# Kernel tuning notes

Hardware: AMD Instinct MI355X
Metric: run time of the kernel (lower is better)

Reference implementation:

```python
import jax, jax.numpy as jnp
import numpy as np

B = 16        # graphs per batch
NPG = 4096    # nodes per graph
N = B * NPG
EPG = 32768   # edges per graph
E = B * EPG
F_NODE, F_EDGE, G, H, A = 8, 4, 16, 128, 10


def setup_inputs() -> dict:
    key = jax.random.key(0)
    ks = jax.random.split(key, 32)
    x = jax.random.normal(ks[0], (N, F_NODE), jnp.float32)
    # random intra-graph edges, offset into the batched node id space
    src = jax.random.randint(ks[1], (B, EPG), 0, NPG)
    dst = jax.random.randint(ks[2], (B, EPG), 0, NPG)
    off = (jnp.arange(B) * NPG)[:, None]
    edge_index = jnp.stack([(src + off).reshape(-1), (dst + off).reshape(-1)]).astype(jnp.int64)
    edge_attr = jax.random.normal(ks[3], (E, F_EDGE), jnp.float32)
    global_state = jax.random.normal(ks[4], (B, G), jnp.float32)
    current_pipe_nodes = jax.random.randint(ks[5], (B, 2), 0, NPG).astype(jnp.int64)

    def w(k, shape):
        fan_in = shape[0] if len(shape) > 1 else shape[0]
        return jax.random.normal(k, shape, jnp.float32) * (1.0 / np.sqrt(fan_in))

    return dict(
        x=x, edge_index=edge_index, edge_attr=edge_attr,
        global_state=global_state, current_pipe_nodes=current_pipe_nodes,
        W_l1=w(ks[6], (F_NODE, H)), W_r1=w(ks[7], (F_NODE, H)), W_e1=w(ks[8], (F_EDGE, H)),
        att1=w(ks[9], (H,)), b1=jnp.zeros((H,), jnp.float32),
        W_l2=w(ks[10], (H, H)), W_r2=w(ks[11], (H, H)), W_e2=w(ks[12], (F_EDGE, H)),
        att2=w(ks[13], (H,)), b2=jnp.zeros((H,), jnp.float32),
        W_c=w(ks[14], (H + 2 * H + G, 256)), b_c=jnp.zeros((256,), jnp.float32),
        W_a1=w(ks[15], (256, 128)), b_a1=jnp.zeros((128,), jnp.float32),
        W_a2=w(ks[16], (128, A)), b_a2=jnp.zeros((A,), jnp.float32),
        W_v1=w(ks[17], (256, 128)), b_v1=jnp.zeros((128,), jnp.float32),
        W_v2=w(ks[18], (128, 1)), b_v2=jnp.zeros((1,), jnp.float32),
    )


def add_self_loops(edge_index, edge_attr, n):
    # PyG default: add_self_loops=True, fill_value='mean' -> loop attr is the
    # mean of incoming edge_attr per node (zeros if none).
    dst = edge_index[1]
    deg = jax.ops.segment_sum(jnp.ones(dst.shape, jnp.float32), dst, num_segments=n)
    loop_attr = jax.ops.segment_sum(edge_attr, dst, num_segments=n) / jnp.maximum(deg, 1.0)[:, None]
    loops = jnp.tile(jnp.arange(n, dtype=edge_index.dtype)[None, :], (2, 1))
    ei = jnp.concatenate([edge_index, loops], axis=1)
    ea = jnp.concatenate([edge_attr, loop_attr], axis=0)
    return ei, ea


def gatv2(x, ei, ea, Wl, Wr, We, att, bias, n):
    # GATv2Conv (heads=1): score = att . leaky_relu(Wl x_j + Wr x_i + We e_ij)
    # message = alpha_ij * (Wl x_j); segment softmax over incoming edges of i.
    src, dst = ei[0], ei[1]
    xl = x @ Wl                                   # [N,H]
    xr = x @ Wr                                   # [N,H]
    m = xl[src] + xr[dst] + ea @ We               # [E,H]
    s = jax.nn.leaky_relu(m, 0.2) @ att           # [E]
    smax = jax.ops.segment_max(s, dst, num_segments=n)
    ealpha = jnp.exp(s - smax[dst])
    denom = jax.ops.segment_sum(ealpha, dst, num_segments=n)
    alpha = ealpha / denom[dst]
    out = jax.ops.segment_sum(alpha[:, None] * xl[src], dst, num_segments=n)
    return out + bias


def reference(x, edge_index, edge_attr, global_state, current_pipe_nodes,
              W_l1, W_r1, W_e1, att1, b1,
              W_l2, W_r2, W_e2, att2, b2,
              W_c, b_c, W_a1, b_a1, W_a2, b_a2, W_v1, b_v1, W_v2, b_v2):
    ei, ea = add_self_loops(edge_index, edge_attr, N)
    h = jax.nn.relu(gatv2(x, ei, ea, W_l1, W_r1, W_e1, att1, b1, N))
    h = gatv2(h, ei, ea, W_l2, W_r2, W_e2, att2, b2, N)
    # global_mean_pool: graphs are contiguous equal-size blocks
    graph_emb = h.reshape(B, NPG, H).mean(axis=1)                       # [B,H]
    abs_idx = current_pipe_nodes + (jnp.arange(B) * NPG)[:, None]       # [B,2]
    pipe_emb = h[abs_idx.reshape(-1)].reshape(B, 2 * H)                 # [B,2H]
    comb = jnp.concatenate([graph_emb, pipe_emb, global_state], axis=1)
    feat = jax.nn.relu(comb @ W_c + b_c)
    logits = jax.nn.relu(feat @ W_a1 + b_a1) @ W_a2 + b_a2              # [B,A]
    value = jax.nn.relu(feat @ W_v1 + b_v1) @ W_v2 + b_v2               # [B,1]
    return jnp.concatenate([logits, value], axis=1)                     # [B,A+1]
```

## Files before the change

kernel.cpp:

```cpp
#include <hip/hip_runtime.h>
#include <math.h>

#define NN   65536
#define NPG  4096
#define NB   16
#define NE   524288
#define EPG  32768
#define SB   8
#define NH   128
#define FN   8
#define FE   4
#define NG   16
#define NA   10
#define NFRAG 2048

typedef __attribute__((ext_vector_type(8))) short bf16x8;
typedef __attribute__((ext_vector_type(4))) float f32x4;

static __device__ __forceinline__ short bf16rne(float f) {
    unsigned u = __builtin_bit_cast(unsigned, f);
    u += 0x7FFFu + ((u >> 16) & 1u);
    return (short)(u >> 16);
}

__global__ void hist_lin1_kernel(const int* __restrict__ ei, int* __restrict__ subhist,
                                 const float* __restrict__ x,
                                 const float* __restrict__ Wl, const float* __restrict__ Wr,
                                 float* __restrict__ xl, float* __restrict__ xr) {
    int bid = blockIdx.x;
    if (bid < NB * SB) {
        __shared__ int hh[NPG];
        int g = bid >> 3, sb = bid & 7;
        int t = threadIdx.x;
        for (int i = t; i < NPG; i += 256) hh[i] = 0;
        __syncthreads();
        const int* dstp = ei + NE + g * EPG + sb * (EPG / SB);
        for (int i = t; i < EPG / SB; i += 256)
            atomicAdd(&hh[dstp[i] - g * NPG], 1);
        __syncthreads();
        int* out = subhist + (size_t)bid * NPG;
        for (int i = t; i < NPG; i += 256) out[i] = hh[i];
    } else {
        __shared__ float row[2][FN];
        int b2 = bid - NB * SB;
        int sub = threadIdx.x >> 7;
        int k = threadIdx.x & 127;
        int n = b2 * 2 + sub;
        if (k < FN) row[sub][k] = x[n * FN + k];
        __syncthreads();
        float al = 0.f, ar = 0.f;
#pragma unroll
        for (int j = 0; j < FN; ++j) {
            float v = row[sub][j];
            al += v * Wl[j * NH + k];
            ar += v * Wr[j * NH + k];
        }
        xl[n * NH + k] = al;
        xr[n * NH + k] = ar;
    }
}

__global__ __launch_bounds__(1024) void scan_kernel(
        const int* __restrict__ subhist, int* __restrict__ offs, int* __restrict__ cur2,
        const float* __restrict__ Wl2, const float* __restrict__ Wr2,
        bf16x8* __restrict__ wbf) {
    int g = blockIdx.x, t = threadIdx.x;
    if (g >= NB) {
        int sel = g - NB;
        const float* W = sel ? Wr2 : Wl2;
#pragma unroll
        for (int q = 0; q < 2; ++q) {
            int f = t * 2 + q;
            int lane = f & 63;
            int kgct = f >> 6;
            int kg = kgct & 3, ct = kgct >> 2;
            int kbase = kg * 32 + (lane >> 4) * 8;
            int c = ct * 16 + (lane & 15);
            bf16x8 v;
#pragma unroll
            for (int j = 0; j < 8; ++j)
                v[j] = bf16rne(W[(kbase + j) * NH + c]);
            wbf[sel * NFRAG + f] = v;
        }
        return;
    }
    __shared__ int psum[1024];
    int h[4][SB];
    int loc[4];
    int run = 0;
#pragma unroll
    for (int i = 0; i < 4; ++i) {
        int nl = t * 4 + i;
        int d = 0;
#pragma unroll
        for (int sb = 0; sb < SB; ++sb) {
            int v = subhist[((size_t)(g * SB + sb)) * NPG + nl];
            h[i][sb] = v;
            d += v;
        }
        loc[i] = run;
        run += d;
    }
    psum[t] = run;
    __syncthreads();
    for (int s = 1; s < 1024; s <<= 1) {
        int add = (t >= s) ? psum[t - s] : 0;
        __syncthreads();
        psum[t] += add;
        __syncthreads();
    }
    int prefix = (t == 0) ? 0 : psum[t - 1];
    int ebase = g * EPG;
#pragma unroll
    for (int i = 0; i < 4; ++i) {
        int nl = t * 4 + i;
        int off = ebase + prefix + loc[i];
        offs[g * NPG + nl] = off;
        int running = off;
#pragma unroll
        for (int sb = 0; sb < SB; ++sb) {
            cur2[((size_t)(g * SB + sb)) * NPG + nl] = running;
            running += h[i][sb];
        }
    }
    if (g == NB - 1 && t == 0) offs[NN] = NE;
}

__global__ __launch_bounds__(1024) void csr_fill_kernel(
        const int* __restrict__ ei, const int* __restrict__ cur2, int2* __restrict__ csr) {
    __shared__ int cur[NPG];
    int bid = blockIdx.x;
    int g = bid >> 3, sb = bid & 7;
    int t = threadIdx.x;
    const int* base = cur2 + (size_t)bid * NPG;
    for (int i = t; i < NPG; i += 1024) cur[i] = base[i];
    __syncthreads();
    int e0 = g * EPG + sb * (EPG / SB);
#pragma unroll
    for (int i = 0; i < (EPG / SB) / 1024; ++i) {
        int e = e0 + i * 1024 + t;
        int dst = ei[NE + e];
        int src = ei[e];
        int pos = atomicAdd(&cur[dst - g * NPG], 1);
        csr[pos] = make_int2(src, e);
    }
}

__global__ __launch_bounds__(256) void gat_gather_kernel(
        const float4* __restrict__ xl, const float4* __restrict__ xr,
        const float4* __restrict__ ea,
        const int2* __restrict__ csr, const int* __restrict__ offs,
        const float* __restrict__ We, const float* __restrict__ att,
        const float* __restrict__ bias, float* __restrict__ out,
        unsigned short* __restrict__ hbf_out,
        float4* __restrict__ lattr_w, const float4* __restrict__ lattr_r,
        float4* __restrict__ gpart, int do_relu) {
    __shared__ float4 red[8][32];
    int grp = threadIdx.x >> 5;
    int lane = threadIdx.x & 31;
    int bid = blockIdx.x;
    int xcd = bid & 7, slot = bid >> 3;
    int g = xcd + ((slot >> 9) << 3);
    int blk = slot & 511;
    int node = g * NPG + blk * 8 + grp;

    float4 xr4 = xr[node * 32 + lane];
    float4 att4 = ((const float4*)att)[lane];
    const float4* We4 = (const float4*)We;
    float4 we0 = We4[lane];
    float4 we1 = We4[32 + lane];
    float4 we2 = We4[64 + lane];
    float4 we3 = We4[96 + lane];

    int beg = offs[node], end = offs[node + 1];
    float l = 0.f;
    float4 acc = make_float4(0.f, 0.f, 0.f, 0.f);
    float4 easum = make_float4(0.f, 0.f, 0.f, 0.f);
    bool have_lattr = (lattr_r != nullptr);
    if (beg < end) {
        int last = end - 1;
        int2 se0 = csr[beg];
        int p1 = (beg + 1 <= last) ? beg + 1 : last;
        int2 se1 = csr[p1];
        float4 xl0 = xl[se0.x * 32 + lane];
        float4 a0 = ea[se0.y];
        for (int p = beg; p < end; ++p) {
            int p2 = (p + 2 <= last) ? p + 2 : last;
            int2 se2 = csr[p2];
            float4 xl1 = xl[se1.x * 32 + lane];
            float4 a1 = ea[se1.y];
            if (!have_lattr) {
                easum.x += a0.x; easum.y += a0.y; easum.z += a0.z; easum.w += a0.w;
            }
            float tx = xl0.x + xr4.x + a0.x * we0.x + a0.y * we1.x + a0.z * we2.x + a0.w * we3.x;
            float ty = xl0.y + xr4.y + a0.x * we0.y + a0.y * we1.y + a0.z * we2.y + a0.w * we3.y;
            float tz = xl0.z + xr4.z + a0.x * we0.z + a0.y * we1.z + a0.z * we2.z + a0.w * we3.z;
            float tw = xl0.w + xr4.w + a0.x * we0.w + a0.y * we1.w + a0.z * we2.w + a0.w * we3.w;
            tx = tx > 0.f ? tx : 0.2f * tx;
            ty = ty > 0.f ? ty : 0.2f * ty;
            tz = tz > 0.f ? tz : 0.2f * tz;
            tw = tw > 0.f ? tw : 0.2f * tw;
            float s = tx * att4.x + ty * att4.y + tz * att4.z + tw * att4.w;
#pragma unroll
            for (int o = 16; o >= 1; o >>= 1) s += __shfl_xor(s, o);
            float w = __expf(s);
            l += w;
            acc.x += w * xl0.x;
            acc.y += w * xl0.y;
            acc.z += w * xl0.z;
            acc.w += w * xl0.w;
            se1 = se2; xl0 = xl1; a0 = a1;
        }
    }
    {
        float ax, ay, az, aw;
        if (have_lattr) {
            float4 la = lattr_r[node];
            ax = la.x; ay = la.y; az = la.z; aw = la.w;
        } else {
            int deg = end - beg;
            float invd = 1.0f / (float)(deg > 0 ? deg : 1);
            ax = easum.x * invd; ay = easum.y * invd;
            az = easum.z * invd; aw = easum.w * invd;
            if (lane == 0) lattr_w[node] = make_float4(ax, ay, az, aw);
        }
        float4 xl4 = xl[node * 32 + lane];
        float tx = xl4.x + xr4.x + ax * we0.x + ay * we1.x + az * we2.x + aw * we3.x;
        float ty = xl4.y + xr4.y + ax * we0.y + ay * we1.y + az * we2.y + aw * we3.y;
        float tz = xl4.z + xr4.z + ax * we0.z + ay * we1.z + az * we2.z + aw * we3.z;
        float tw = xl4.w + xr4.w + ax * we0.w + ay * we1.w + az * we2.w + aw * we3.w;
        tx = tx > 0.f ? tx : 0.2f * tx;
        ty = ty > 0.f ? ty : 0.2f * ty;
        tz = tz > 0.f ? tz : 0.2f * tz;
        tw = tw > 0.f ? tw : 0.2f * tw;
        float s = tx * att4.x + ty * att4.y + tz * att4.z + tw * att4.w;
#pragma unroll
        for (int o = 16; o >= 1; o >>= 1) s += __shfl_xor(s, o);
        float w = __expf(s);
        l += w;
        acc.x += w * xl4.x;
        acc.y += w * xl4.y;
        acc.z += w * xl4.z;
        acc.w += w * xl4.w;
    }
    float inv = 1.0f / l;
    float4 b4 = ((const float4*)bias)[lane];
    float4 o4;
    o4.x = acc.x * inv + b4.x;
    o4.y = acc.y * inv + b4.y;
    o4.z = acc.z * inv + b4.z;
    o4.w = acc.w * inv + b4.w;
    if (do_relu) {
        o4.x = fmaxf(o4.x, 0.f); o4.y = fmaxf(o4.y, 0.f);
        o4.z = fmaxf(o4.z, 0.f); o4.w = fmaxf(o4.w, 0.f);
    }
    if (hbf_out != nullptr) {
        int rt = node >> 4, m = node & 15;
        int kg = lane >> 3, qd = (lane & 7) >> 1, j0 = (lane & 1) * 4;
        ushort4 v;
        v.x = (unsigned short)bf16rne(o4.x);
        v.y = (unsigned short)bf16rne(o4.y);
        v.z = (unsigned short)bf16rne(o4.z);
        v.w = (unsigned short)bf16rne(o4.w);
        *(ushort4*)&hbf_out[(size_t)(((rt * 4 + kg) * 64 + qd * 16 + m)) * 8 + j0] = v;
    } else {
        ((float4*)out)[node * 32 + lane] = o4;
    }

    if (gpart != nullptr) {
        red[grp][lane] = o4;
        __syncthreads();
        if (grp < 4) {
            float4 o = red[grp + 4][lane];
            red[grp][lane] = make_float4(red[grp][lane].x + o.x, red[grp][lane].y + o.y,
                                         red[grp][lane].z + o.z, red[grp][lane].w + o.w);
        }
        __syncthreads();
        if (grp < 2) {
            float4 o = red[grp + 2][lane];
            red[grp][lane] = make_float4(red[grp][lane].x + o.x, red[grp][lane].y + o.y,
                                         red[grp][lane].z + o.z, red[grp][lane].w + o.w);
        }
        __syncthreads();
        if (grp == 0) {
            float4 a = red[0][lane], b = red[1][lane];
            gpart[(g * 512 + blk) * 32 + lane] =
                make_float4(a.x + b.x, a.y + b.y, a.z + b.z, a.w + b.w);
        }
    }
}

__global__ __launch_bounds__(256) void lin2_mfma_kernel(
        const bf16x8* __restrict__ hbf, const bf16x8* __restrict__ wbf,
        float* __restrict__ xl, float* __restrict__ xr) {
    const bf16x8* Bf = wbf + (size_t)blockIdx.y * NFRAG;
    float* C = blockIdx.y ? xr : xl;
    int t = threadIdx.x;
    int wv = t >> 6, lane = t & 63;
    int rt = blockIdx.x * 4 + wv;
    int row0 = rt * 16;
    int m = lane & 15, qd = lane >> 4;
    bf16x8 afrag[4];
#pragma unroll
    for (int kg = 0; kg < 4; ++kg)
        afrag[kg] = hbf[(size_t)(rt * 4 + kg) * 64 + lane];
#pragma unroll
    for (int ct = 0; ct < 8; ++ct) {
        f32x4 acc = {0.f, 0.f, 0.f, 0.f};
#pragma unroll
        for (int kg = 0; kg < 4; ++kg) {
            bf16x8 b = Bf[((ct << 2) | kg) * 64 + lane];
            acc = __builtin_amdgcn_mfma_f32_16x16x32_bf16(afrag[kg], b, acc, 0, 0, 0);
        }
        int col = ct * 16 + m;
#pragma unroll
        for (int r = 0; r < 4; ++r)
            C[(size_t)(row0 + qd * 4 + r) * NH + col] = acc[r];
    }
}

__global__ __launch_bounds__(1024) void head_kernel(
        const float* __restrict__ gpart, const float* __restrict__ h,
        const float* __restrict__ gstate, const int* __restrict__ cpn,
        const float* __restrict__ Wc, const float* __restrict__ bc,
        const float* __restrict__ Wa1, const float* __restrict__ ba1,
        const float* __restrict__ Wa2, const float* __restrict__ ba2,
        const float* __restrict__ Wv1, const float* __restrict__ bv1,
        const float* __restrict__ Wv2, const float* __restrict__ bv2,
        float* __restrict__ out) {
    int b = blockIdx.x, t = threadIdx.x;
    __shared__ float comb[400];
    __shared__ float part[4][256];
    __shared__ float pp[8][128];
    __shared__ float feat[256];
    __shared__ float hid[256];
    int n0 = cpn[b * 2 + 0] + b * NPG;
    int n1 = cpn[b * 2 + 1] + b * NPG;
    {
        int d = t & 127, p = t >> 7;
        const float* gp = gpart + (size_t)b * 512 * NH + d;
        float s = 0.f;
        int c0 = p * 64;
        for (int c = c0; c < c0 + 64; ++c) s += gp[c * NH];
        pp[p][d] = s;
    }
    if (t >= 128 && t < 256) comb[128 + (t - 128)] = h[(size_t)n0 * NH + (t - 128)];
    else if (t >= 256 && t < 384) comb[t] = h[(size_t)n1 * NH + (t - 256)];
    else if (t >= 384 && t < 400) comb[t] = gstate[b * NG + (t - 384)];
    __syncthreads();
    if (t < 128) {
        float s = pp[0][t] + pp[1][t] + pp[2][t] + pp[3][t]
                + pp[4][t] + pp[5][t] + pp[6][t] + pp[7][t];
        comb[t] = s * (1.0f / NPG);
    }
    __syncthreads();
    {
        int col = t & 255, p = t >> 8;
        float a = 0.f;
        int j0 = p * 100;
        for (int j = j0; j < j0 + 100; ++j) a += comb[j] * Wc[j * 256 + col];
        part[p][col] = a;
    }
    __syncthreads();
    if (t < 256)
        feat[t] = fmaxf(bc[t] + part[0][t] + part[1][t] + part[2][t] + part[3][t], 0.f);
    __syncthreads();
    {
        int col = t & 255, p = t >> 8;
        const float* W = (col < 128) ? Wa1 : Wv1;
        int cc = col & 127;
        float a = 0.f;
        int j0 = p * 64;
        for (int j = j0; j < j0 + 64; ++j) a += feat[j] * W[j * 128 + cc];
        part[p][col] = a;
    }
    __syncthreads();
    if (t < 256) {
        float bias = (t < 128) ? ba1[t] : bv1[t - 128];
        hid[t] = fmaxf(bias + part[0][t] + part[1][t] + part[2][t] + part[3][t], 0.f);
    }
    __syncthreads();
    if (t < NA) {
        float a2 = ba2[t];
        for (int j = 0; j < NH; ++j) a2 += hid[j] * Wa2[j * NA + t];
        out[b * 11 + t] = a2;
    } else if (t == NA) {
        float a2 = bv2[0];
        for (int j = 0; j < NH; ++j) a2 += hid[128 + j] * Wv2[j];
        out[b * 11 + 10] = a2;
    }
}

extern "C" void kernel_launch(void* const* d_in, const int* in_sizes, int n_in,
                              void* d_out, int out_size, void* d_ws, size_t ws_size,
                              hipStream_t stream) {
    const float* x      = (const float*)d_in[0];
    const int*   ei     = (const int*)d_in[1];
    const float* ea     = (const float*)d_in[2];
    const float* gstate = (const float*)d_in[3];
    const int*   cpn    = (const int*)d_in[4];
    const float* Wl1 = (const float*)d_in[5];
    const float* Wr1 = (const float*)d_in[6];
    const float* We1 = (const float*)d_in[7];
    const float* att1= (const float*)d_in[8];
    const float* b1  = (const float*)d_in[9];
    const float* Wl2 = (const float*)d_in[10];
    const float* Wr2 = (const float*)d_in[11];
    const float* We2 = (const float*)d_in[12];
    const float* att2= (const float*)d_in[13];
    const float* b2  = (const float*)d_in[14];
    const float* Wc  = (const float*)d_in[15];
    const float* bc  = (const float*)d_in[16];
    const float* Wa1 = (const float*)d_in[17];
    const float* ba1 = (const float*)d_in[18];
    const float* Wa2 = (const float*)d_in[19];
    const float* ba2 = (const float*)d_in[20];
    const float* Wv1 = (const float*)d_in[21];
    const float* bv1 = (const float*)d_in[22];
    const float* Wv2 = (const float*)d_in[23];
    const float* bv2 = (const float*)d_in[24];

    char* ws = (char*)d_ws;
    size_t o = 0;
    float* xl     = (float*)(ws + o); o += (size_t)NN * NH * 4;
    float* xr     = (float*)(ws + o); o += (size_t)NN * NH * 4;
    float* h      = (float*)(ws + o); o += (size_t)NN * NH * 4;
    unsigned short* hbf = (unsigned short*)(ws + o); o += (size_t)NN * NH * 2;
    float* lattr  = (float*)(ws + o); o += (size_t)NN * 16;
    float* gpart  = (float*)(ws + o); o += (size_t)NB * 512 * NH * 4;
    int*   offs   = (int*)(ws + o);   o += (((size_t)(NN + 1) * 4 + 255) & ~(size_t)255);
    int*   subhist= (int*)(ws + o);   o += (size_t)NB * SB * NPG * 4;
    int*   cur2   = (int*)(ws + o);   o += (size_t)NB * SB * NPG * 4;
    int2*  csr    = (int2*)(ws + o);  o += (size_t)NE * 8;
    bf16x8* wbf   = (bf16x8*)(ws + o); o += (size_t)2 * NFRAG * 16;
    (void)o; (void)ws_size; (void)in_sizes; (void)n_in; (void)out_size;

    hist_lin1_kernel<<<NB * SB + NN / 2, 256, 0, stream>>>(ei, subhist, x, Wl1, Wr1, xl, xr);
    scan_kernel<<<NB + 2, 1024, 0, stream>>>(subhist, offs, cur2, Wl2, Wr2, wbf);
    csr_fill_kernel<<<NB * SB, 1024, 0, stream>>>(ei, cur2, csr);
    gat_gather_kernel<<<NN / 8, 256, 0, stream>>>((const float4*)xl, (const float4*)xr,
        (const float4*)ea, csr, offs, We1, att1, b1, nullptr, hbf,
        (float4*)lattr, nullptr, nullptr, 1);
    lin2_mfma_kernel<<<dim3(NN / 64, 2), 256, 0, stream>>>((const bf16x8*)hbf, wbf, xl, xr);
    gat_gather_kernel<<<NN / 8, 256, 0, stream>>>((const float4*)xl, (const float4*)xr,
        (const float4*)ea, csr, offs, We2, att2, b2, h, nullptr,
        nullptr, (const float4*)lattr, (float4*)gpart, 0);
    head_kernel<<<NB, 1024, 0, stream>>>(gpart, h, gstate, cpn, Wc, bc, Wa1, ba1, Wa2, ba2,
                                         Wv1, bv1, Wv2, bv2, (float*)d_out);
}
```

Measured before the change: 296.2 us.

## Fuse scan into CSR fill, move weight packing, write only pipe-node rows

Removes the separate scan kernel. Each csr_fill block now recomputes its graph's prefix scan and its own sub-block cursor offsets, and the bf16 weight packing moves into two extra blocks of the histogram kernel. The second GAT layer no longer writes the full 32 MB fp32 h array. It stores only the two pipe-node rows per graph, which the head kernel reads. This trades one launch and a large global write for redundant scan work (8x per graph) inside csr_fill.

```diff
diff --git a/kernel.cpp b/kernel.cpp
--- a/kernel.cpp
+++ b/kernel.cpp
@@ -26,6 +26,8 @@
 __global__ void hist_lin1_kernel(const int* __restrict__ ei, int* __restrict__ subhist,
                                  const float* __restrict__ x,
                                  const float* __restrict__ Wl, const float* __restrict__ Wr,
+                                 const float* __restrict__ Wl2, const float* __restrict__ Wr2,
+                                 bf16x8* __restrict__ wbf,
                                  float* __restrict__ xl, float* __restrict__ xr) {
     int bid = blockIdx.x;
     if (bid < NB * SB) {
@@ -40,37 +42,13 @@
         __syncthreads();
         int* out = subhist + (size_t)bid * NPG;
         for (int i = t; i < NPG; i += 256) out[i] = hh[i];
-    } else {
-        __shared__ float row[2][FN];
-        int b2 = bid - NB * SB;
-        int sub = threadIdx.x >> 7;
-        int k = threadIdx.x & 127;
-        int n = b2 * 2 + sub;
-        if (k < FN) row[sub][k] = x[n * FN + k];
-        __syncthreads();
-        float al = 0.f, ar = 0.f;
-#pragma unroll
-        for (int j = 0; j < FN; ++j) {
-            float v = row[sub][j];
-            al += v * Wl[j * NH + k];
-            ar += v * Wr[j * NH + k];
-        }
-        xl[n * NH + k] = al;
-        xr[n * NH + k] = ar;
-    }
-}
-
-__global__ __launch_bounds__(1024) void scan_kernel(
-        const int* __restrict__ subhist, int* __restrict__ offs, int* __restrict__ cur2,
-        const float* __restrict__ Wl2, const float* __restrict__ Wr2,
-        bf16x8* __restrict__ wbf) {
-    int g = blockIdx.x, t = threadIdx.x;
-    if (g >= NB) {
-        int sel = g - NB;
+    } else if (bid < NB * SB + 2) {
+        int sel = bid - NB * SB;
         const float* W = sel ? Wr2 : Wl2;
-#pragma unroll
-        for (int q = 0; q < 2; ++q) {
-            int f = t * 2 + q;
+        int t = threadIdx.x;
+#pragma unroll
+        for (int q = 0; q < 8; ++q) {
+            int f = t * 8 + q;
             int lane = f & 63;
             int kgct = f >> 6;
             int kg = kgct & 3, ct = kgct >> 2;
@@ -82,58 +60,69 @@
                 v[j] = bf16rne(W[(kbase + j) * NH + c]);
             wbf[sel * NFRAG + f] = v;
         }
-        return;
-    }
+    } else {
+        __shared__ float row[2][FN];
+        int b2 = bid - NB * SB - 2;
+        int sub = threadIdx.x >> 7;
+        int k = threadIdx.x & 127;
+        int n = b2 * 2 + sub;
+        if (k < FN) row[sub][k] = x[n * FN + k];
+        __syncthreads();
+        float al = 0.f, ar = 0.f;
+#pragma unroll
+        for (int j = 0; j < FN; ++j) {
+            float v = row[sub][j];
+            al += v * Wl[j * NH + k];
+            ar += v * Wr[j * NH + k];
+        }
+        xl[n * NH + k] = al;
+        xr[n * NH + k] = ar;
+    }
+}
+
+__global__ __launch_bounds__(1024) void csr_fill_kernel(
+        const int* __restrict__ ei, const int* __restrict__ subhist,
+        int* __restrict__ offs, int2* __restrict__ csr) {
+    __shared__ int cur[NPG];
     __shared__ int psum[1024];
-    int h[4][SB];
-    int loc[4];
-    int run = 0;
-#pragma unroll
-    for (int i = 0; i < 4; ++i) {
-        int nl = t * 4 + i;
-        int d = 0;
-#pragma unroll
-        for (int sb = 0; sb < SB; ++sb) {
-            int v = subhist[((size_t)(g * SB + sb)) * NPG + nl];
-            h[i][sb] = v;
-            d += v;
-        }
-        loc[i] = run;
-        run += d;
-    }
-    psum[t] = run;
-    __syncthreads();
-    for (int s = 1; s < 1024; s <<= 1) {
-        int add = (t >= s) ? psum[t - s] : 0;
-        __syncthreads();
-        psum[t] += add;
-        __syncthreads();
-    }
-    int prefix = (t == 0) ? 0 : psum[t - 1];
-    int ebase = g * EPG;
-#pragma unroll
-    for (int i = 0; i < 4; ++i) {
-        int nl = t * 4 + i;
-        int off = ebase + prefix + loc[i];
-        offs[g * NPG + nl] = off;
-        int running = off;
-#pragma unroll
-        for (int sb = 0; sb < SB; ++sb) {
-            cur2[((size_t)(g * SB + sb)) * NPG + nl] = running;
-            running += h[i][sb];
-        }
-    }
-    if (g == NB - 1 && t == 0) offs[NN] = NE;
-}
-
-__global__ __launch_bounds__(1024) void csr_fill_kernel(
-        const int* __restrict__ ei, const int* __restrict__ cur2, int2* __restrict__ csr) {
-    __shared__ int cur[NPG];
     int bid = blockIdx.x;
     int g = bid >> 3, sb = bid & 7;
     int t = threadIdx.x;
-    const int* base = cur2 + (size_t)bid * NPG;
-    for (int i = t; i < NPG; i += 1024) cur[i] = base[i];
+    int base4 = t * 4;
+    int dpre[4], loc[4];
+    int run = 0;
+#pragma unroll
+    for (int i = 0; i < 4; ++i) {
+        int nl = base4 + i;
+        int d = 0, pre = 0;
+#pragma unroll
+        for (int s = 0; s < SB; ++s) {
+            int v = subhist[((size_t)(g * SB + s)) * NPG + nl];
+            pre += (s < sb) ? v : 0;
+            d += v;
+        }
+        dpre[i] = pre;
+        loc[i] = run;
+        run += d;
+    }
+    psum[t] = run;
+    __syncthreads();
+    for (int s = 1; s < 1024; s <<= 1) {
+        int add = (t >= s) ? psum[t - s] : 0;
+        __syncthreads();
+        psum[t] += add;
+        __syncthreads();
+    }
+    int prefix = (t == 0) ? 0 : psum[t - 1];
+    int ebase = g * EPG;
+#pragma unroll
+    for (int i = 0; i < 4; ++i) {
+        int nl = base4 + i;
+        int off = ebase + prefix + loc[i];
+        cur[nl] = off + dpre[i];
+        if (sb == 0) offs[g * NPG + nl] = off;
+    }
+    if (sb == 0 && g == NB - 1 && t == 0) offs[NN] = NE;
     __syncthreads();
     int e0 = g * EPG + sb * (EPG / SB);
 #pragma unroll
@@ -151,10 +140,11 @@
         const float4* __restrict__ ea,
         const int2* __restrict__ csr, const int* __restrict__ offs,
         const float* __restrict__ We, const float* __restrict__ att,
-        const float* __restrict__ bias, float* __restrict__ out,
+        const float* __restrict__ bias,
         unsigned short* __restrict__ hbf_out,
         float4* __restrict__ lattr_w, const float4* __restrict__ lattr_r,
-        float4* __restrict__ gpart, int do_relu) {
+        float4* __restrict__ gpart, float4* __restrict__ pipe,
+        const int* __restrict__ cpn, int do_relu) {
     __shared__ float4 red[8][32];
     int grp = threadIdx.x >> 5;
     int lane = threadIdx.x & 31;
@@ -264,7 +254,9 @@
         v.w = (unsigned short)bf16rne(o4.w);
         *(ushort4*)&hbf_out[(size_t)(((rt * 4 + kg) * 64 + qd * 16 + m)) * 8 + j0] = v;
     } else {
-        ((float4*)out)[node * 32 + lane] = o4;
+        int nl = node - g * NPG;
+        if (nl == cpn[g * 2 + 0]) pipe[(g * 2 + 0) * 32 + lane] = o4;
+        if (nl == cpn[g * 2 + 1]) pipe[(g * 2 + 1) * 32 + lane] = o4;
     }
 
     if (gpart != nullptr) {
@@ -320,8 +312,8 @@
 }
 
 __global__ __launch_bounds__(1024) void head_kernel(
-        const float* __restrict__ gpart, const float* __restrict__ h,
-        const float* __restrict__ gstate, const int* __restrict__ cpn,
+        const float* __restrict__ gpart, const float* __restrict__ pipe,
+        const float* __restrict__ gstate,
         const float* __restrict__ Wc, const float* __restrict__ bc,
         const float* __restrict__ Wa1, const float* __restrict__ ba1,
         const float* __restrict__ Wa2, const float* __restrict__ ba2,
@@ -334,8 +326,6 @@
     __shared__ float pp[8][128];
     __shared__ float feat[256];
     __shared__ float hid[256];
-    int n0 = cpn[b * 2 + 0] + b * NPG;
-    int n1 = cpn[b * 2 + 1] + b * NPG;
     {
         int d = t & 127, p = t >> 7;
         const float* gp = gpart + (size_t)b * 512 * NH + d;
@@ -344,8 +334,7 @@
         for (int c = c0; c < c0 + 64; ++c) s += gp[c * NH];
         pp[p][d] = s;
     }
-    if (t >= 128 && t < 256) comb[128 + (t - 128)] = h[(size_t)n0 * NH + (t - 128)];
-    else if (t >= 256 && t < 384) comb[t] = h[(size_t)n1 * NH + (t - 256)];
+    if (t >= 128 && t < 384) comb[t] = pipe[(size_t)b * 2 * NH + (t - 128)];
     else if (t >= 384 && t < 400) comb[t] = gstate[b * NG + (t - 384)];
     __syncthreads();
     if (t < 128) {
@@ -424,27 +413,26 @@
     size_t o = 0;
     float* xl     = (float*)(ws + o); o += (size_t)NN * NH * 4;
     float* xr     = (float*)(ws + o); o += (size_t)NN * NH * 4;
-    float* h      = (float*)(ws + o); o += (size_t)NN * NH * 4;
     unsigned short* hbf = (unsigned short*)(ws + o); o += (size_t)NN * NH * 2;
     float* lattr  = (float*)(ws + o); o += (size_t)NN * 16;
     float* gpart  = (float*)(ws + o); o += (size_t)NB * 512 * NH * 4;
+    float* pipe   = (float*)(ws + o); o += (size_t)NB * 2 * NH * 4;
     int*   offs   = (int*)(ws + o);   o += (((size_t)(NN + 1) * 4 + 255) & ~(size_t)255);
     int*   subhist= (int*)(ws + o);   o += (size_t)NB * SB * NPG * 4;
-    int*   cur2   = (int*)(ws + o);   o += (size_t)NB * SB * NPG * 4;
     int2*  csr    = (int2*)(ws + o);  o += (size_t)NE * 8;
     bf16x8* wbf   = (bf16x8*)(ws + o); o += (size_t)2 * NFRAG * 16;
     (void)o; (void)ws_size; (void)in_sizes; (void)n_in; (void)out_size;
 
-    hist_lin1_kernel<<<NB * SB + NN / 2, 256, 0, stream>>>(ei, subhist, x, Wl1, Wr1, xl, xr);
-    scan_kernel<<<NB + 2, 1024, 0, stream>>>(subhist, offs, cur2, Wl2, Wr2, wbf);
-    csr_fill_kernel<<<NB * SB, 1024, 0, stream>>>(ei, cur2, csr);
+    hist_lin1_kernel<<<NB * SB + 2 + NN / 2, 256, 0, stream>>>(ei, subhist, x, Wl1, Wr1,
+                                                               Wl2, Wr2, wbf, xl, xr);
+    csr_fill_kernel<<<NB * SB, 1024, 0, stream>>>(ei, subhist, offs, csr);
     gat_gather_kernel<<<NN / 8, 256, 0, stream>>>((const float4*)xl, (const float4*)xr,
-        (const float4*)ea, csr, offs, We1, att1, b1, nullptr, hbf,
-        (float4*)lattr, nullptr, nullptr, 1);
+        (const float4*)ea, csr, offs, We1, att1, b1, hbf,
+        (float4*)lattr, nullptr, nullptr, nullptr, cpn, 1);
     lin2_mfma_kernel<<<dim3(NN / 64, 2), 256, 0, stream>>>((const bf16x8*)hbf, wbf, xl, xr);
     gat_gather_kernel<<<NN / 8, 256, 0, stream>>>((const float4*)xl, (const float4*)xr,
-        (const float4*)ea, csr, offs, We2, att2, b2, h, nullptr,
-        nullptr, (const float4*)lattr, (float4*)gpart, 0);
-    head_kernel<<<NB, 1024, 0, stream>>>(gpart, h, gstate, cpn, Wc, bc, Wa1, ba1, Wa2, ba2,
+        (const float4*)ea, csr, offs, We2, att2, b2, nullptr,
+        nullptr, (const float4*)lattr, (float4*)gpart, (float4*)pipe, cpn, 0);
+    head_kernel<<<NB, 1024, 0, stream>>>(gpart, pipe, gstate, Wc, bc, Wa1, ba1, Wa2, ba2,
                                          Wv1, bv1, Wv2, bv2, (float*)d_out);
 }
```

Result: no change. 292.0 us (-1.4%).
